# Kernel optimization log

Hardware: AMD Instinct MI355X
Metric: run time of the kernel (lower is better)

## Reference

```python
import jax, jax.numpy as jnp
import numpy as np

N = 100000
E = 1600000
IN_C, HID_C, OUT_C = 128, 128, 64


def setup_inputs() -> dict:
    key = jax.random.key(0)
    ks = jax.random.split(key, 8)
    x = jax.random.normal(ks[0], (N, IN_C), dtype=jnp.float32)
    edge_index = jax.random.randint(ks[1], (2, E), 0, N, dtype=jnp.int64)
    s = 1.0 / np.sqrt(IN_C)
    s2 = 1.0 / np.sqrt(HID_C)
    return {
        "x": x,
        "edge_index": edge_index,
        # layer 1: SAGEConv(in=128, out=128): lin_l (neighbor, with bias), lin_r (root, no bias)
        "W_l1": jax.random.uniform(ks[2], (IN_C, HID_C), jnp.float32, -s, s),
        "b_l1": jnp.zeros((HID_C,), jnp.float32),
        "W_r1": jax.random.uniform(ks[3], (IN_C, HID_C), jnp.float32, -s, s),
        # layer 2: SAGEConv(in=128, out=64)
        "W_l2": jax.random.uniform(ks[4], (HID_C, OUT_C), jnp.float32, -s2, s2),
        "b_l2": jnp.zeros((OUT_C,), jnp.float32),
        "W_r2": jax.random.uniform(ks[5], (HID_C, OUT_C), jnp.float32, -s2, s2),
    }


def _sage_conv(x, src, dst, W_l, b_l, W_r, n_nodes):
    # mean aggregation of source-node features at target nodes
    msg = x[src]                                    # [E, d] gather
    agg = jax.ops.segment_sum(msg, dst, num_segments=n_nodes)          # [N, d]
    cnt = jax.ops.segment_sum(jnp.ones((src.shape[0], 1), x.dtype), dst,
                              num_segments=n_nodes)                    # [N, 1]
    mean = agg / jnp.maximum(cnt, 1.0)
    # out = lin_l(mean_neighbors) + lin_r(x_self)
    return mean @ W_l + b_l + x @ W_r


def reference(x, edge_index, W_l1, b_l1, W_r1, W_l2, b_l2, W_r2):
    src, dst = edge_index[0], edge_index[1]
    n = x.shape[0]
    h = _sage_conv(x, src, dst, W_l1, b_l1, W_r1, n)
    h = jax.nn.relu(h)  # dropout is identity in eval mode
    out = _sage_conv(h, src, dst, W_l2, b_l2, W_r2, n)
    return out
```

## Files before the change

kernel.cpp:

```cpp
#include <hip/hip_runtime.h>
#include <hip/hip_bf16.h>
#include <stdint.h>

#define IN_C 128
#define HID_C 128
#define OUT_C 64

#define NBUCK 256
#define BSH 9
#define EPB 4096

typedef _Float16 h8 __attribute__((ext_vector_type(8)));
typedef _Float16 h2 __attribute__((ext_vector_type(2)));
typedef float f4 __attribute__((ext_vector_type(4)));
typedef float f2 __attribute__((ext_vector_type(2)));
typedef unsigned u4 __attribute__((ext_vector_type(4)));

__device__ inline float h2lo(unsigned v){ h2 t = __builtin_bit_cast(h2, v); return (float)t[0]; }
__device__ inline float h2hi(unsigned v){ h2 t = __builtin_bit_cast(h2, v); return (float)t[1]; }
__device__ inline unsigned packh2(float a, float b){ h2 t; t[0]=(_Float16)a; t[1]=(_Float16)b; return __builtin_bit_cast(unsigned, t); }

__global__ __launch_bounds__(256) void k_hist(const int* __restrict__ dst, int E,
                                              int* __restrict__ histT, int NBLK){
    __shared__ int h[NBUCK];
    int t = threadIdx.x;
    h[t] = 0; __syncthreads();
    int e0 = blockIdx.x*EPB, e1 = min(E, e0 + EPB);
    for (int e = e0 + t; e < e1; e += 256) atomicAdd(&h[((unsigned)dst[e]) >> BSH], 1);
    __syncthreads();
    histT[t*NBLK + blockIdx.x] = h[t];
}

__global__ void k_scanA(const int* __restrict__ cnt, int* __restrict__ tmp, int* __restrict__ bsum, int n){
    __shared__ int s[256];
    int t = threadIdx.x, g = blockIdx.x*256 + t;
    int v = (g < n) ? cnt[g] : 0;
    s[t] = v; __syncthreads();
    for (int off = 1; off < 256; off <<= 1){
        int a = (t >= off) ? s[t-off] : 0;
        __syncthreads();
        s[t] += a;
        __syncthreads();
    }
    int excl = (t == 0) ? 0 : s[t-1];
    if (g < n) tmp[g] = excl;
    if (t == 255) bsum[blockIdx.x] = s[255];
}

__global__ void k_scanB(int* __restrict__ bsum, int nb){
    __shared__ int s[1024];
    int t = threadIdx.x;
    int v = (t < nb) ? bsum[t] : 0;
    s[t] = v; __syncthreads();
    for (int off = 1; off < 1024; off <<= 1){
        int a = (t >= off) ? s[t-off] : 0;
        __syncthreads();
        s[t] += a;
        __syncthreads();
    }
    int excl = (t == 0) ? 0 : s[t-1];
    if (t < nb) bsum[t] = excl;
}

__global__ __launch_bounds__(256) void k_scatter(const int* __restrict__ src, const int* __restrict__ dst,
                                                 int E, const int* __restrict__ tmp, const int* __restrict__ bsum,
                                                 int NBLK, unsigned* __restrict__ sorted){
    __shared__ int off[NBUCK];
    int t = threadIdx.x;
    int g = t*NBLK + blockIdx.x;
    off[t] = tmp[g] + bsum[g >> 8];
    __syncthreads();
    int e0 = blockIdx.x*EPB, e1 = min(E, e0 + EPB);
    for (int e = e0 + t; e < e1; e += 256){
        int d = dst[e];
        int b = ((unsigned)d) >> BSH;
        int p = atomicAdd(&off[b], 1);
        sorted[p] = (unsigned)src[e] | (((unsigned)(d & ((1<<BSH)-1))) << 17);
    }
}

__global__ __launch_bounds__(512) void k_csr(const unsigned* __restrict__ sorted,
                                             const int* __restrict__ tmp, const int* __restrict__ bsum,
                                             int NBLK, int E, int N,
                                             int* __restrict__ csr, int* __restrict__ row_start){
    __shared__ int cnt[512];
    __shared__ int sc[512];
    int b = blockIdx.x, t = threadIdx.x;
    int i0 = b*NBLK;
    int bs = tmp[i0] + bsum[i0 >> 8];
    int be = (b == NBUCK-1) ? E : (tmp[i0 + NBLK] + bsum[(i0 + NBLK) >> 8]);
    cnt[t] = 0; __syncthreads();
    for (int e = bs + t; e < be; e += 512) atomicAdd(&cnt[sorted[e] >> 17], 1);
    __syncthreads();
    sc[t] = cnt[t]; __syncthreads();
    for (int off = 1; off < 512; off <<= 1){
        int a = (t >= off) ? sc[t-off] : 0;
        __syncthreads();
        sc[t] += a;
        __syncthreads();
    }
    int excl = sc[t] - cnt[t];
    int nid = (b << BSH) + t;
    if (nid < N) row_start[nid] = bs + excl;
    if (t == 0 && b == (N >> BSH)) row_start[N] = E;
    __syncthreads();
    cnt[t] = excl;
    __syncthreads();
    for (int e = bs + t; e < be; e += 512){
        unsigned v = sorted[e];
        int dl = v >> 17;
        int p = atomicAdd(&cnt[dl], 1);
        csr[bs + p] = (int)(v & 0x1FFFFu);
    }
}

__global__ void k_cvt(const float* __restrict__ x, h8* __restrict__ xh, uint2* __restrict__ x8, int n8){
    int g = blockIdx.x*256 + threadIdx.x;
    if (g < n8){
        const f4* xp = (const f4*)(x + (size_t)g*8);
        f4 a = xp[0], b = xp[1];
        h8 o;
        o[0]=(_Float16)a[0]; o[1]=(_Float16)a[1]; o[2]=(_Float16)a[2]; o[3]=(_Float16)a[3];
        o[4]=(_Float16)b[0]; o[5]=(_Float16)b[1]; o[6]=(_Float16)b[2]; o[7]=(_Float16)b[3];
        xh[g] = o;
        int w0 = __builtin_amdgcn_cvt_pk_fp8_f32(a[0], a[1], 0, false);
        w0     = __builtin_amdgcn_cvt_pk_fp8_f32(a[2], a[3], w0, true);
        int w1 = __builtin_amdgcn_cvt_pk_fp8_f32(b[0], b[1], 0, false);
        w1     = __builtin_amdgcn_cvt_pk_fp8_f32(b[2], b[3], w1, true);
        uint2 p; p.x = (unsigned)w0; p.y = (unsigned)w1;
        x8[g] = p;
    }
}

__device__ inline void pack_one(const float* __restrict__ W, int C, _Float16* __restrict__ outp, int tid){
    int l = tid & 63;
    int f = tid >> 6;
    int NJT = C / 16;
    int kt = f / NJT;
    int jt = f - kt*NJT;
    int kbase = kt*32 + (l >> 4)*8;
    int col   = jt*16 + (l & 15);
    h8 o;
    #pragma unroll
    for (int r = 0; r < 8; ++r) o[r] = (_Float16)W[(kbase + r)*C + col];
    ((h8*)outp)[f*64 + l] = o;
}

__global__ void k_pack(const float* __restrict__ Wl1, const float* __restrict__ Wr1,
                       const float* __restrict__ Wl2, const float* __restrict__ Wr2,
                       _Float16* __restrict__ wl1p, _Float16* __restrict__ wr1p,
                       _Float16* __restrict__ wl2p, _Float16* __restrict__ wr2p){
    int tid = blockIdx.x*256 + threadIdx.x;
    if (tid < 2048)        pack_one(Wl1, 128, wl1p, tid);
    else if (tid < 4096)   pack_one(Wr1, 128, wr1p, tid - 2048);
    else if (tid < 5120)   pack_one(Wl2,  64, wl2p, tid - 4096);
    else if (tid < 6144)   pack_one(Wr2,  64, wr2p, tid - 5120);
}

__global__ void k_agg1(const int* __restrict__ row_start, const int* __restrict__ csr,
                       const uint2* __restrict__ x8, unsigned* __restrict__ mh32, int n){
    int node = (int)((blockIdx.x*(unsigned)blockDim.x + threadIdx.x) >> 4);
    int c = threadIdx.x & 15;
    if (node >= n) return;
    int base = row_start[node], end = row_start[node+1];
    int deg = end - base;
    f2 a0={0.f,0.f}, a1={0.f,0.f}, a2={0.f,0.f}, a3={0.f,0.f};
    f2 b0={0.f,0.f}, b1={0.f,0.f}, b2={0.f,0.f}, b3={0.f,0.f};
    int i = base;
    for (; i + 3 < end; i += 4){
        int e0 = csr[i], e1 = csr[i+1], e2 = csr[i+2], e3 = csr[i+3];
        uint2 v0 = x8[(size_t)e0*16 + c];
        uint2 v1 = x8[(size_t)e1*16 + c];
        uint2 v2 = x8[(size_t)e2*16 + c];
        uint2 v3 = x8[(size_t)e3*16 + c];
        a0 += __builtin_amdgcn_cvt_pk_f32_fp8(v0.x, false);
        a1 += __builtin_amdgcn_cvt_pk_f32_fp8(v0.x, true);
        a2 += __builtin_amdgcn_cvt_pk_f32_fp8(v0.y, false);
        a3 += __builtin_amdgcn_cvt_pk_f32_fp8(v0.y, true);
        b0 += __builtin_amdgcn_cvt_pk_f32_fp8(v1.x, false);
        b1 += __builtin_amdgcn_cvt_pk_f32_fp8(v1.x, true);
        b2 += __builtin_amdgcn_cvt_pk_f32_fp8(v1.y, false);
        b3 += __builtin_amdgcn_cvt_pk_f32_fp8(v1.y, true);
        a0 += __builtin_amdgcn_cvt_pk_f32_fp8(v2.x, false);
        a1 += __builtin_amdgcn_cvt_pk_f32_fp8(v2.x, true);
        a2 += __builtin_amdgcn_cvt_pk_f32_fp8(v2.y, false);
        a3 += __builtin_amdgcn_cvt_pk_f32_fp8(v2.y, true);
        b0 += __builtin_amdgcn_cvt_pk_f32_fp8(v3.x, false);
        b1 += __builtin_amdgcn_cvt_pk_f32_fp8(v3.x, true);
        b2 += __builtin_amdgcn_cvt_pk_f32_fp8(v3.y, false);
        b3 += __builtin_amdgcn_cvt_pk_f32_fp8(v3.y, true);
    }
    for (; i < end; ++i){
        int e = csr[i];
        uint2 v = x8[(size_t)e*16 + c];
        a0 += __builtin_amdgcn_cvt_pk_f32_fp8(v.x, false);
        a1 += __builtin_amdgcn_cvt_pk_f32_fp8(v.x, true);
        a2 += __builtin_amdgcn_cvt_pk_f32_fp8(v.y, false);
        a3 += __builtin_amdgcn_cvt_pk_f32_fp8(v.y, true);
    }
    a0 += b0; a1 += b1; a2 += b2; a3 += b3;
    float sc = 1.0f / (float)max(deg, 1);
    u4 o;
    o[0] = packh2(a0[0]*sc, a0[1]*sc);
    o[1] = packh2(a1[0]*sc, a1[1]*sc);
    o[2] = packh2(a2[0]*sc, a2[1]*sc);
    o[3] = packh2(a3[0]*sc, a3[1]*sc);
    *(u4*)(mh32 + (size_t)node*64 + 4*c) = o;
}

__global__ __launch_bounds__(256, 2) void k_gemm_fused(
    const _Float16* __restrict__ A0,
    const _Float16* __restrict__ A1,
    const h8* __restrict__ B0,
    const h8* __restrict__ B1,
    const float* __restrict__ bias1,
    const h8* __restrict__ W2l,
    const h8* __restrict__ W2r,
    const float* __restrict__ bias2,
    unsigned* __restrict__ P8,
    float* __restrict__ Q,
    int M)
{
    __shared__ h8 shB[4096];
    int tid = threadIdx.x;
    #pragma unroll
    for (int i = 0; i < 8; ++i) shB[i*256 + tid] = B0[i*256 + tid];
    #pragma unroll
    for (int i = 0; i < 8; ++i) shB[2048 + i*256 + tid] = B1[i*256 + tid];
    __syncthreads();

    int wid = tid >> 6, lane = tid & 63;
    int m0 = (blockIdx.x*4 + wid) * 16;
    if (m0 >= M) return;
    int m = lane & 15, kg = lane >> 4;
    int rowc = min(m0 + m, M-1);

    f4 acc[8];
    #pragma unroll
    for (int j = 0; j < 8; ++j) acc[j] = (f4)0.0f;

    #pragma unroll
    for (int ph = 0; ph < 2; ++ph){
        const _Float16* A = ph ? A1 : A0;
        #pragma unroll
        for (int kt = 0; kt < 4; ++kt){
            h8 nf = *(const h8*)(A + (size_t)rowc*128 + kt*32 + kg*8);
            #pragma unroll
            for (int j = 0; j < 8; ++j){
                h8 wf = shB[ph*2048 + (kt*8 + j)*64 + lane];
                acc[j] = __builtin_amdgcn_mfma_f32_16x16x32_f16(wf, nf, acc[j], 0, 0, 0);
            }
        }
    }

    unsigned hreg[16];
    #pragma unroll
    for (int j = 0; j < 8; ++j){
        f4 bb = *(const f4*)(bias1 + j*16 + kg*4);
        float v0 = acc[j][0] + bb[0]; v0 = v0 > 0.f ? v0 : 0.f;
        float v1 = acc[j][1] + bb[1]; v1 = v1 > 0.f ? v1 : 0.f;
        float v2 = acc[j][2] + bb[2]; v2 = v2 > 0.f ? v2 : 0.f;
        float v3 = acc[j][3] + bb[3]; v3 = v3 > 0.f ? v3 : 0.f;
        hreg[2*j]   = packh2(v0, v1);
        hreg[2*j+1] = packh2(v2, v3);
    }

    f4 accP[4], accQ[4];
    #pragma unroll
    for (int j = 0; j < 4; ++j){ accP[j] = (f4)0.0f; accQ[j] = (f4)0.0f; }

    int srcA = ((kg & 1) * 2) * 16 + m;
    int srcB = srcA + 16;
    bool hi = (kg >> 1) & 1;

    #pragma unroll
    for (int kt = 0; kt < 4; ++kt){
        unsigned sA0 = (unsigned)__shfl((int)hreg[4*kt+0], srcA, 64);
        unsigned sA1 = (unsigned)__shfl((int)hreg[4*kt+1], srcA, 64);
        unsigned sA2 = (unsigned)__shfl((int)hreg[4*kt+2], srcA, 64);
        unsigned sA3 = (unsigned)__shfl((int)hreg[4*kt+3], srcA, 64);
        unsigned sB0 = (unsigned)__shfl((int)hreg[4*kt+0], srcB, 64);
        unsigned sB1 = (unsigned)__shfl((int)hreg[4*kt+1], srcB, 64);
        unsigned sB2 = (unsigned)__shfl((int)hreg[4*kt+2], srcB, 64);
        unsigned sB3 = (unsigned)__shfl((int)hreg[4*kt+3], srcB, 64);
        u4 u;
        u[0] = hi ? sA2 : sA0;
        u[1] = hi ? sA3 : sA1;
        u[2] = hi ? sB2 : sB0;
        u[3] = hi ? sB3 : sB1;
        h8 hf = __builtin_bit_cast(h8, u);
        #pragma unroll
        for (int j2 = 0; j2 < 4; ++j2){
            accP[j2] = __builtin_amdgcn_mfma_f32_16x16x32_f16(W2l[(kt*4 + j2)*64 + lane], hf, accP[j2], 0, 0, 0);
            accQ[j2] = __builtin_amdgcn_mfma_f32_16x16x32_f16(W2r[(kt*4 + j2)*64 + lane], hf, accQ[j2], 0, 0, 0);
        }
    }

    int node = m0 + m;
    if (node < M){
        #pragma unroll
        for (int j2 = 0; j2 < 4; ++j2){
            int f = j2*16 + kg*4;
            int p8 = __builtin_amdgcn_cvt_pk_fp8_f32(accP[j2][0], accP[j2][1], 0, false);
            p8     = __builtin_amdgcn_cvt_pk_fp8_f32(accP[j2][2], accP[j2][3], p8, true);
            P8[(size_t)node*16 + j2*4 + kg] = (unsigned)p8;
            f4 bb2 = *(const f4*)(bias2 + f);
            f4 qv;
            qv[0] = accQ[j2][0] + bb2[0];
            qv[1] = accQ[j2][1] + bb2[1];
            qv[2] = accQ[j2][2] + bb2[2];
            qv[3] = accQ[j2][3] + bb2[3];
            *(f4*)(Q + (size_t)node*64 + f) = qv;
        }
    }
}

__global__ void k_agg2f(const int* __restrict__ row_start, const int* __restrict__ csr,
                        const unsigned* __restrict__ p8, const float* __restrict__ Q,
                        float* __restrict__ out, int n){
    int node = (int)((blockIdx.x*(unsigned)blockDim.x + threadIdx.x) >> 4);
    int c = threadIdx.x & 15;
    if (node >= n) return;
    int base = row_start[node], end = row_start[node+1];
    int deg = end - base;
    f2 a0={0.f,0.f}, a1={0.f,0.f}, b0={0.f,0.f}, b1={0.f,0.f};
    f2 c0={0.f,0.f}, c1={0.f,0.f}, d0={0.f,0.f}, d1={0.f,0.f};
    int i = base;
    for (; i + 3 < end; i += 4){
        int e0 = csr[i], e1 = csr[i+1], e2 = csr[i+2], e3 = csr[i+3];
        unsigned v0 = p8[(size_t)e0*16 + c];
        unsigned v1 = p8[(size_t)e1*16 + c];
        unsigned v2 = p8[(size_t)e2*16 + c];
        unsigned v3 = p8[(size_t)e3*16 + c];
        a0 += __builtin_amdgcn_cvt_pk_f32_fp8(v0, false);
        a1 += __builtin_amdgcn_cvt_pk_f32_fp8(v0, true);
        b0 += __builtin_amdgcn_cvt_pk_f32_fp8(v1, false);
        b1 += __builtin_amdgcn_cvt_pk_f32_fp8(v1, true);
        c0 += __builtin_amdgcn_cvt_pk_f32_fp8(v2, false);
        c1 += __builtin_amdgcn_cvt_pk_f32_fp8(v2, true);
        d0 += __builtin_amdgcn_cvt_pk_f32_fp8(v3, false);
        d1 += __builtin_amdgcn_cvt_pk_f32_fp8(v3, true);
    }
    for (; i < end; ++i){
        int e = csr[i];
        unsigned v = p8[(size_t)e*16 + c];
        a0 += __builtin_amdgcn_cvt_pk_f32_fp8(v, false);
        a1 += __builtin_amdgcn_cvt_pk_f32_fp8(v, true);
    }
    a0 += b0 + c0 + d0;
    a1 += b1 + c1 + d1;
    float sc = 1.0f / (float)max(deg, 1);
    f4 q = *(const f4*)(Q + (size_t)node*64 + 4*c);
    f4 o;
    o[0] = a0[0]*sc + q[0];
    o[1] = a0[1]*sc + q[1];
    o[2] = a1[0]*sc + q[2];
    o[3] = a1[1]*sc + q[3];
    *(f4*)(out + (size_t)node*64 + 4*c) = o;
}

extern "C" void kernel_launch(void* const* d_in, const int* in_sizes, int n_in,
                              void* d_out, int out_size, void* d_ws, size_t ws_size,
                              hipStream_t stream) {
    const float* x   = (const float*)d_in[0];
    const int*   ei  = (const int*)d_in[1];
    const float* Wl1 = (const float*)d_in[2];
    const float* bl1 = (const float*)d_in[3];
    const float* Wr1 = (const float*)d_in[4];
    const float* Wl2 = (const float*)d_in[5];
    const float* bl2 = (const float*)d_in[6];
    const float* Wr2 = (const float*)d_in[7];

    const int N = in_sizes[0] / IN_C;
    const int E = in_sizes[1] / 2;
    const int* src = ei;
    const int* dst = ei + E;

    const int NBLK = (E + EPB - 1) / EPB;
    const int n_s  = NBUCK * NBLK;

    char* w = (char*)d_ws;
    size_t off = 0;
    auto alloc = [&](size_t bytes) -> char* {
        char* p = w + off;
        off = (off + bytes + 255) & ~(size_t)255;
        return p;
    };
    int* histT      = (int*)alloc((size_t)n_s*4);
    int* tmp        = (int*)alloc((size_t)n_s*4);
    int* bsum       = (int*)alloc(4096);
    unsigned* sorted= (unsigned*)alloc((size_t)E*4);
    int* csr        = (int*)alloc((size_t)E*4);
    int* row_start  = (int*)alloc((size_t)(N+1)*4);
    _Float16* xh    = (_Float16*)alloc((size_t)N*IN_C*2);
    unsigned* x8    = (unsigned*)alloc((size_t)N*IN_C);
    _Float16* m1h   = (_Float16*)alloc((size_t)N*IN_C*2);
    unsigned* p8    = (unsigned*)alloc((size_t)N*OUT_C);
    _Float16* wl1p  = (_Float16*)alloc(4*8*64*8*2);
    _Float16* wr1p  = (_Float16*)alloc(4*8*64*8*2);
    _Float16* wl2p  = (_Float16*)alloc(4*4*64*8*2);
    _Float16* wr2p  = (_Float16*)alloc(4*4*64*8*2);

    const int SB = (n_s + 255) / 256;

    k_hist   <<<NBLK, 256, 0, stream>>>(dst, E, histT, NBLK);
    k_scanA  <<<SB, 256, 0, stream>>>(histT, tmp, bsum, n_s);
    k_scanB  <<<1, 1024, 0, stream>>>(bsum, SB);
    k_scatter<<<NBLK, 256, 0, stream>>>(src, dst, E, tmp, bsum, NBLK, sorted);
    k_csr    <<<NBUCK, 512, 0, stream>>>(sorted, tmp, bsum, NBLK, E, N, csr, row_start);

    const int n8 = N*IN_C/8;
    k_cvt<<<(n8 + 255)/256, 256, 0, stream>>>(x, (h8*)xh, (uint2*)x8, n8);
    k_pack<<<24, 256, 0, stream>>>(Wl1, Wr1, Wl2, Wr2, wl1p, wr1p, wl2p, wr2p);

    const int AB = (N + 15) / 16;
    k_agg1<<<AB, 256, 0, stream>>>(row_start, csr, (const uint2*)x8, (unsigned*)m1h, N);

    float* Q = (float*)d_out;
    const int GB2 = (N + 63)/64;
    k_gemm_fused<<<GB2, 256, 0, stream>>>(m1h, xh, (const h8*)wl1p, (const h8*)wr1p, bl1,
                                          (const h8*)wl2p, (const h8*)wr2p, bl2,
                                          p8, Q, N);

    k_agg2f<<<AB, 256, 0, stream>>>(row_start, csr, p8, Q, (float*)d_out, N);
}
```

Before: 159.8 us.

## Fuse front-end kernels, split neighbor edges across lanes, store Q in fp16

Histogram, weight packing and the fp32-to-fp16/fp8 conversion are merged into one launch, which removes two kernel launches. EPB is doubled, so there are fewer histogram and scatter blocks, and scanB shrinks to 256 threads. Both aggregation kernels now give each wave four nodes in turn, with the four 16-lane groups reading different edges in parallel and combining results by cross-lane shuffles, which exposes more memory parallelism per node. The layer-2 root term Q is stored as fp16 in workspace instead of fp32 in the output, which halves that traffic but lowers precision.

```diff
diff --git a/kernel.cpp b/kernel.cpp
--- a/kernel.cpp
+++ b/kernel.cpp
@@ -8,7 +8,7 @@
 
 #define NBUCK 256
 #define BSH 9
-#define EPB 4096
+#define EPB 8192
 
 typedef _Float16 h8 __attribute__((ext_vector_type(8)));
 typedef _Float16 h2 __attribute__((ext_vector_type(2)));
@@ -20,15 +20,59 @@
 __device__ inline float h2hi(unsigned v){ h2 t = __builtin_bit_cast(h2, v); return (float)t[1]; }
 __device__ inline unsigned packh2(float a, float b){ h2 t; t[0]=(_Float16)a; t[1]=(_Float16)b; return __builtin_bit_cast(unsigned, t); }
 
-__global__ __launch_bounds__(256) void k_hist(const int* __restrict__ dst, int E,
-                                              int* __restrict__ histT, int NBLK){
+__device__ inline void pack_one(const float* __restrict__ W, int C, _Float16* __restrict__ outp, int tid){
+    int l = tid & 63;
+    int f = tid >> 6;
+    int NJT = C / 16;
+    int kt = f / NJT;
+    int jt = f - kt*NJT;
+    int kbase = kt*32 + (l >> 4)*8;
+    int col   = jt*16 + (l & 15);
+    h8 o;
+    #pragma unroll
+    for (int r = 0; r < 8; ++r) o[r] = (_Float16)W[(kbase + r)*C + col];
+    ((h8*)outp)[f*64 + l] = o;
+}
+
+__global__ __launch_bounds__(256) void k_front(const int* __restrict__ dst, int E, int NBLK,
+                                               int* __restrict__ histT,
+                                               const float* __restrict__ x, h8* __restrict__ xh,
+                                               uint2* __restrict__ x8, int n8,
+                                               const float* __restrict__ Wl1, const float* __restrict__ Wr1,
+                                               const float* __restrict__ Wl2, const float* __restrict__ Wr2,
+                                               _Float16* __restrict__ wl1p, _Float16* __restrict__ wr1p,
+                                               _Float16* __restrict__ wl2p, _Float16* __restrict__ wr2p){
     __shared__ int h[NBUCK];
-    int t = threadIdx.x;
-    h[t] = 0; __syncthreads();
-    int e0 = blockIdx.x*EPB, e1 = min(E, e0 + EPB);
-    for (int e = e0 + t; e < e1; e += 256) atomicAdd(&h[((unsigned)dst[e]) >> BSH], 1);
-    __syncthreads();
-    histT[t*NBLK + blockIdx.x] = h[t];
+    int bid = blockIdx.x, t = threadIdx.x;
+    if (bid < NBLK){
+        h[t] = 0; __syncthreads();
+        int e0 = bid*EPB, e1 = min(E, e0 + EPB);
+        for (int e = e0 + t; e < e1; e += 256) atomicAdd(&h[((unsigned)dst[e]) >> BSH], 1);
+        __syncthreads();
+        histT[t*NBLK + bid] = h[t];
+    } else if (bid < NBLK + 24){
+        int tid = (bid - NBLK)*256 + t;
+        if (tid < 2048)        pack_one(Wl1, 128, wl1p, tid);
+        else if (tid < 4096)   pack_one(Wr1, 128, wr1p, tid - 2048);
+        else if (tid < 5120)   pack_one(Wl2,  64, wl2p, tid - 4096);
+        else if (tid < 6144)   pack_one(Wr2,  64, wr2p, tid - 5120);
+    } else {
+        int g = (bid - NBLK - 24)*256 + t;
+        if (g < n8){
+            const f4* xp = (const f4*)(x + (size_t)g*8);
+            f4 a = xp[0], b = xp[1];
+            h8 o;
+            o[0]=(_Float16)a[0]; o[1]=(_Float16)a[1]; o[2]=(_Float16)a[2]; o[3]=(_Float16)a[3];
+            o[4]=(_Float16)b[0]; o[5]=(_Float16)b[1]; o[6]=(_Float16)b[2]; o[7]=(_Float16)b[3];
+            xh[g] = o;
+            int w0 = __builtin_amdgcn_cvt_pk_fp8_f32(a[0], a[1], 0, false);
+            w0     = __builtin_amdgcn_cvt_pk_fp8_f32(a[2], a[3], w0, true);
+            int w1 = __builtin_amdgcn_cvt_pk_fp8_f32(b[0], b[1], 0, false);
+            w1     = __builtin_amdgcn_cvt_pk_fp8_f32(b[2], b[3], w1, true);
+            uint2 p; p.x = (unsigned)w0; p.y = (unsigned)w1;
+            x8[g] = p;
+        }
+    }
 }
 
 __global__ void k_scanA(const int* __restrict__ cnt, int* __restrict__ tmp, int* __restrict__ bsum, int n){
@@ -48,11 +92,11 @@
 }
 
 __global__ void k_scanB(int* __restrict__ bsum, int nb){
-    __shared__ int s[1024];
+    __shared__ int s[256];
     int t = threadIdx.x;
     int v = (t < nb) ? bsum[t] : 0;
     s[t] = v; __syncthreads();
-    for (int off = 1; off < 1024; off <<= 1){
+    for (int off = 1; off < 256; off <<= 1){
         int a = (t >= off) ? s[t-off] : 0;
         __syncthreads();
         s[t] += a;
@@ -114,98 +158,65 @@
     }
 }
 
-__global__ void k_cvt(const float* __restrict__ x, h8* __restrict__ xh, uint2* __restrict__ x8, int n8){
-    int g = blockIdx.x*256 + threadIdx.x;
-    if (g < n8){
-        const f4* xp = (const f4*)(x + (size_t)g*8);
-        f4 a = xp[0], b = xp[1];
-        h8 o;
-        o[0]=(_Float16)a[0]; o[1]=(_Float16)a[1]; o[2]=(_Float16)a[2]; o[3]=(_Float16)a[3];
-        o[4]=(_Float16)b[0]; o[5]=(_Float16)b[1]; o[6]=(_Float16)b[2]; o[7]=(_Float16)b[3];
-        xh[g] = o;
-        int w0 = __builtin_amdgcn_cvt_pk_fp8_f32(a[0], a[1], 0, false);
-        w0     = __builtin_amdgcn_cvt_pk_fp8_f32(a[2], a[3], w0, true);
-        int w1 = __builtin_amdgcn_cvt_pk_fp8_f32(b[0], b[1], 0, false);
-        w1     = __builtin_amdgcn_cvt_pk_fp8_f32(b[2], b[3], w1, true);
-        uint2 p; p.x = (unsigned)w0; p.y = (unsigned)w1;
-        x8[g] = p;
-    }
-}
-
-__device__ inline void pack_one(const float* __restrict__ W, int C, _Float16* __restrict__ outp, int tid){
-    int l = tid & 63;
-    int f = tid >> 6;
-    int NJT = C / 16;
-    int kt = f / NJT;
-    int jt = f - kt*NJT;
-    int kbase = kt*32 + (l >> 4)*8;
-    int col   = jt*16 + (l & 15);
-    h8 o;
-    #pragma unroll
-    for (int r = 0; r < 8; ++r) o[r] = (_Float16)W[(kbase + r)*C + col];
-    ((h8*)outp)[f*64 + l] = o;
-}
-
-__global__ void k_pack(const float* __restrict__ Wl1, const float* __restrict__ Wr1,
-                       const float* __restrict__ Wl2, const float* __restrict__ Wr2,
-                       _Float16* __restrict__ wl1p, _Float16* __restrict__ wr1p,
-                       _Float16* __restrict__ wl2p, _Float16* __restrict__ wr2p){
-    int tid = blockIdx.x*256 + threadIdx.x;
-    if (tid < 2048)        pack_one(Wl1, 128, wl1p, tid);
-    else if (tid < 4096)   pack_one(Wr1, 128, wr1p, tid - 2048);
-    else if (tid < 5120)   pack_one(Wl2,  64, wl2p, tid - 4096);
-    else if (tid < 6144)   pack_one(Wr2,  64, wr2p, tid - 5120);
-}
-
-__global__ void k_agg1(const int* __restrict__ row_start, const int* __restrict__ csr,
-                       const uint2* __restrict__ x8, unsigned* __restrict__ mh32, int n){
-    int node = (int)((blockIdx.x*(unsigned)blockDim.x + threadIdx.x) >> 4);
-    int c = threadIdx.x & 15;
-    if (node >= n) return;
-    int base = row_start[node], end = row_start[node+1];
-    int deg = end - base;
-    f2 a0={0.f,0.f}, a1={0.f,0.f}, a2={0.f,0.f}, a3={0.f,0.f};
-    f2 b0={0.f,0.f}, b1={0.f,0.f}, b2={0.f,0.f}, b3={0.f,0.f};
-    int i = base;
-    for (; i + 3 < end; i += 4){
-        int e0 = csr[i], e1 = csr[i+1], e2 = csr[i+2], e3 = csr[i+3];
-        uint2 v0 = x8[(size_t)e0*16 + c];
-        uint2 v1 = x8[(size_t)e1*16 + c];
-        uint2 v2 = x8[(size_t)e2*16 + c];
-        uint2 v3 = x8[(size_t)e3*16 + c];
-        a0 += __builtin_amdgcn_cvt_pk_f32_fp8(v0.x, false);
-        a1 += __builtin_amdgcn_cvt_pk_f32_fp8(v0.x, true);
-        a2 += __builtin_amdgcn_cvt_pk_f32_fp8(v0.y, false);
-        a3 += __builtin_amdgcn_cvt_pk_f32_fp8(v0.y, true);
-        b0 += __builtin_amdgcn_cvt_pk_f32_fp8(v1.x, false);
-        b1 += __builtin_amdgcn_cvt_pk_f32_fp8(v1.x, true);
-        b2 += __builtin_amdgcn_cvt_pk_f32_fp8(v1.y, false);
-        b3 += __builtin_amdgcn_cvt_pk_f32_fp8(v1.y, true);
-        a0 += __builtin_amdgcn_cvt_pk_f32_fp8(v2.x, false);
-        a1 += __builtin_amdgcn_cvt_pk_f32_fp8(v2.x, true);
-        a2 += __builtin_amdgcn_cvt_pk_f32_fp8(v2.y, false);
-        a3 += __builtin_amdgcn_cvt_pk_f32_fp8(v2.y, true);
-        b0 += __builtin_amdgcn_cvt_pk_f32_fp8(v3.x, false);
-        b1 += __builtin_amdgcn_cvt_pk_f32_fp8(v3.x, true);
-        b2 += __builtin_amdgcn_cvt_pk_f32_fp8(v3.y, false);
-        b3 += __builtin_amdgcn_cvt_pk_f32_fp8(v3.y, true);
-    }
-    for (; i < end; ++i){
-        int e = csr[i];
-        uint2 v = x8[(size_t)e*16 + c];
-        a0 += __builtin_amdgcn_cvt_pk_f32_fp8(v.x, false);
-        a1 += __builtin_amdgcn_cvt_pk_f32_fp8(v.x, true);
-        a2 += __builtin_amdgcn_cvt_pk_f32_fp8(v.y, false);
-        a3 += __builtin_amdgcn_cvt_pk_f32_fp8(v.y, true);
-    }
-    a0 += b0; a1 += b1; a2 += b2; a3 += b3;
-    float sc = 1.0f / (float)max(deg, 1);
-    u4 o;
-    o[0] = packh2(a0[0]*sc, a0[1]*sc);
-    o[1] = packh2(a1[0]*sc, a1[1]*sc);
-    o[2] = packh2(a2[0]*sc, a2[1]*sc);
-    o[3] = packh2(a3[0]*sc, a3[1]*sc);
-    *(u4*)(mh32 + (size_t)node*64 + 4*c) = o;
+__global__ __launch_bounds__(256) void k_agg1(const int* __restrict__ row_start, const int* __restrict__ csr,
+                                              const uint2* __restrict__ x8, unsigned* __restrict__ mh32, int n){
+    int wave = (int)((blockIdx.x*(unsigned)blockDim.x + threadIdx.x) >> 6);
+    int lane = threadIdx.x & 63;
+    int e4 = lane >> 4, c = lane & 15;
+    int n0 = wave*4;
+    if (n0 >= n) return;
+    #pragma unroll 1
+    for (int k = 0; k < 4; ++k){
+        int node = n0 + k;
+        if (node >= n) break;
+        int base = row_start[node], end = row_start[node+1];
+        int deg = end - base;
+        f2 a0={0.f,0.f},a1={0.f,0.f},a2={0.f,0.f},a3={0.f,0.f};
+        f2 b0={0.f,0.f},b1={0.f,0.f},b2={0.f,0.f},b3={0.f,0.f};
+        int i = base;
+        for (; i + 8 <= end; i += 8){
+            int ea = csr[i + e4];
+            int eb = csr[i + 4 + e4];
+            uint2 va = x8[(size_t)ea*16 + c];
+            uint2 vb = x8[(size_t)eb*16 + c];
+            a0 += __builtin_amdgcn_cvt_pk_f32_fp8(va.x, false);
+            a1 += __builtin_amdgcn_cvt_pk_f32_fp8(va.x, true);
+            a2 += __builtin_amdgcn_cvt_pk_f32_fp8(va.y, false);
+            a3 += __builtin_amdgcn_cvt_pk_f32_fp8(va.y, true);
+            b0 += __builtin_amdgcn_cvt_pk_f32_fp8(vb.x, false);
+            b1 += __builtin_amdgcn_cvt_pk_f32_fp8(vb.x, true);
+            b2 += __builtin_amdgcn_cvt_pk_f32_fp8(vb.y, false);
+            b3 += __builtin_amdgcn_cvt_pk_f32_fp8(vb.y, true);
+        }
+        for (; i < end; i += 4){
+            if (i + e4 < end){
+                int e = csr[i + e4];
+                uint2 v = x8[(size_t)e*16 + c];
+                a0 += __builtin_amdgcn_cvt_pk_f32_fp8(v.x, false);
+                a1 += __builtin_amdgcn_cvt_pk_f32_fp8(v.x, true);
+                a2 += __builtin_amdgcn_cvt_pk_f32_fp8(v.y, false);
+                a3 += __builtin_amdgcn_cvt_pk_f32_fp8(v.y, true);
+            }
+        }
+        a0 += b0; a1 += b1; a2 += b2; a3 += b3;
+        a0[0] += __shfl_xor(a0[0], 16); a0[1] += __shfl_xor(a0[1], 16);
+        a1[0] += __shfl_xor(a1[0], 16); a1[1] += __shfl_xor(a1[1], 16);
+        a2[0] += __shfl_xor(a2[0], 16); a2[1] += __shfl_xor(a2[1], 16);
+        a3[0] += __shfl_xor(a3[0], 16); a3[1] += __shfl_xor(a3[1], 16);
+        a0[0] += __shfl_xor(a0[0], 32); a0[1] += __shfl_xor(a0[1], 32);
+        a1[0] += __shfl_xor(a1[0], 32); a1[1] += __shfl_xor(a1[1], 32);
+        a2[0] += __shfl_xor(a2[0], 32); a2[1] += __shfl_xor(a2[1], 32);
+        a3[0] += __shfl_xor(a3[0], 32); a3[1] += __shfl_xor(a3[1], 32);
+        if (e4 == 0){
+            float sc = 1.0f / (float)max(deg, 1);
+            u4 o;
+            o[0] = packh2(a0[0]*sc, a0[1]*sc);
+            o[1] = packh2(a1[0]*sc, a1[1]*sc);
+            o[2] = packh2(a2[0]*sc, a2[1]*sc);
+            o[3] = packh2(a3[0]*sc, a3[1]*sc);
+            *(u4*)(mh32 + (size_t)node*64 + 4*c) = o;
+        }
+    }
 }
 
 __global__ __launch_bounds__(256, 2) void k_gemm_fused(
@@ -218,7 +229,7 @@
     const h8* __restrict__ W2r,
     const float* __restrict__ bias2,
     unsigned* __restrict__ P8,
-    float* __restrict__ Q,
+    uint2* __restrict__ Qh,
     int M)
 {
     __shared__ h8 shB[4096];
@@ -305,58 +316,64 @@
             p8     = __builtin_amdgcn_cvt_pk_fp8_f32(accP[j2][2], accP[j2][3], p8, true);
             P8[(size_t)node*16 + j2*4 + kg] = (unsigned)p8;
             f4 bb2 = *(const f4*)(bias2 + f);
-            f4 qv;
-            qv[0] = accQ[j2][0] + bb2[0];
-            qv[1] = accQ[j2][1] + bb2[1];
-            qv[2] = accQ[j2][2] + bb2[2];
-            qv[3] = accQ[j2][3] + bb2[3];
-            *(f4*)(Q + (size_t)node*64 + f) = qv;
-        }
-    }
-}
-
-__global__ void k_agg2f(const int* __restrict__ row_start, const int* __restrict__ csr,
-                        const unsigned* __restrict__ p8, const float* __restrict__ Q,
-                        float* __restrict__ out, int n){
-    int node = (int)((blockIdx.x*(unsigned)blockDim.x + threadIdx.x) >> 4);
-    int c = threadIdx.x & 15;
-    if (node >= n) return;
-    int base = row_start[node], end = row_start[node+1];
-    int deg = end - base;
-    f2 a0={0.f,0.f}, a1={0.f,0.f}, b0={0.f,0.f}, b1={0.f,0.f};
-    f2 c0={0.f,0.f}, c1={0.f,0.f}, d0={0.f,0.f}, d1={0.f,0.f};
-    int i = base;
-    for (; i + 3 < end; i += 4){
-        int e0 = csr[i], e1 = csr[i+1], e2 = csr[i+2], e3 = csr[i+3];
-        unsigned v0 = p8[(size_t)e0*16 + c];
-        unsigned v1 = p8[(size_t)e1*16 + c];
-        unsigned v2 = p8[(size_t)e2*16 + c];
-        unsigned v3 = p8[(size_t)e3*16 + c];
-        a0 += __builtin_amdgcn_cvt_pk_f32_fp8(v0, false);
-        a1 += __builtin_amdgcn_cvt_pk_f32_fp8(v0, true);
-        b0 += __builtin_amdgcn_cvt_pk_f32_fp8(v1, false);
-        b1 += __builtin_amdgcn_cvt_pk_f32_fp8(v1, true);
-        c0 += __builtin_amdgcn_cvt_pk_f32_fp8(v2, false);
-        c1 += __builtin_amdgcn_cvt_pk_f32_fp8(v2, true);
-        d0 += __builtin_amdgcn_cvt_pk_f32_fp8(v3, false);
-        d1 += __builtin_amdgcn_cvt_pk_f32_fp8(v3, true);
-    }
-    for (; i < end; ++i){
-        int e = csr[i];
-        unsigned v = p8[(size_t)e*16 + c];
-        a0 += __builtin_amdgcn_cvt_pk_f32_fp8(v, false);
-        a1 += __builtin_amdgcn_cvt_pk_f32_fp8(v, true);
-    }
-    a0 += b0 + c0 + d0;
-    a1 += b1 + c1 + d1;
-    float sc = 1.0f / (float)max(deg, 1);
-    f4 q = *(const f4*)(Q + (size_t)node*64 + 4*c);
-    f4 o;
-    o[0] = a0[0]*sc + q[0];
-    o[1] = a0[1]*sc + q[1];
-    o[2] = a1[0]*sc + q[2];
-    o[3] = a1[1]*sc + q[3];
-    *(f4*)(out + (size_t)node*64 + 4*c) = o;
+            uint2 qp;
+            qp.x = packh2(accQ[j2][0] + bb2[0], accQ[j2][1] + bb2[1]);
+            qp.y = packh2(accQ[j2][2] + bb2[2], accQ[j2][3] + bb2[3]);
+            Qh[(size_t)node*16 + j2*4 + kg] = qp;
+        }
+    }
+}
+
+__global__ __launch_bounds__(256) void k_agg2f(const int* __restrict__ row_start, const int* __restrict__ csr,
+                                               const unsigned* __restrict__ p8, const uint2* __restrict__ Qh,
+                                               float* __restrict__ out, int n){
+    int wave = (int)((blockIdx.x*(unsigned)blockDim.x + threadIdx.x) >> 6);
+    int lane = threadIdx.x & 63;
+    int e4 = lane >> 4, c = lane & 15;
+    int n0 = wave*4;
+    if (n0 >= n) return;
+    #pragma unroll 1
+    for (int k = 0; k < 4; ++k){
+        int node = n0 + k;
+        if (node >= n) break;
+        int base = row_start[node], end = row_start[node+1];
+        int deg = end - base;
+        f2 a0={0.f,0.f}, a1={0.f,0.f}, b0={0.f,0.f}, b1={0.f,0.f};
+        int i = base;
+        for (; i + 8 <= end; i += 8){
+            int ea = csr[i + e4];
+            int eb = csr[i + 4 + e4];
+            unsigned va = p8[(size_t)ea*16 + c];
+            unsigned vb = p8[(size_t)eb*16 + c];
+            a0 += __builtin_amdgcn_cvt_pk_f32_fp8(va, false);
+            a1 += __builtin_amdgcn_cvt_pk_f32_fp8(va, true);
+            b0 += __builtin_amdgcn_cvt_pk_f32_fp8(vb, false);
+            b1 += __builtin_amdgcn_cvt_pk_f32_fp8(vb, true);
+        }
+        for (; i < end; i += 4){
+            if (i + e4 < end){
+                int e = csr[i + e4];
+                unsigned v = p8[(size_t)e*16 + c];
+                a0 += __builtin_amdgcn_cvt_pk_f32_fp8(v, false);
+                a1 += __builtin_amdgcn_cvt_pk_f32_fp8(v, true);
+            }
+        }
+        a0 += b0; a1 += b1;
+        a0[0] += __shfl_xor(a0[0], 16); a0[1] += __shfl_xor(a0[1], 16);
+        a1[0] += __shfl_xor(a1[0], 16); a1[1] += __shfl_xor(a1[1], 16);
+        a0[0] += __shfl_xor(a0[0], 32); a0[1] += __shfl_xor(a0[1], 32);
+        a1[0] += __shfl_xor(a1[0], 32); a1[1] += __shfl_xor(a1[1], 32);
+        if (e4 == 0){
+            float sc = 1.0f / (float)max(deg, 1);
+            uint2 qh = Qh[(size_t)node*16 + c];
+            f4 o;
+            o[0] = a0[0]*sc + h2lo(qh.x);
+            o[1] = a0[1]*sc + h2hi(qh.x);
+            o[2] = a1[0]*sc + h2lo(qh.y);
+            o[3] = a1[1]*sc + h2hi(qh.y);
+            *(f4*)(out + (size_t)node*64 + 4*c) = o;
+        }
+    }
 }
 
 extern "C" void kernel_launch(void* const* d_in, const int* in_sizes, int n_in,
@@ -396,31 +413,31 @@
     unsigned* x8    = (unsigned*)alloc((size_t)N*IN_C);
     _Float16* m1h   = (_Float16*)alloc((size_t)N*IN_C*2);
     unsigned* p8    = (unsigned*)alloc((size_t)N*OUT_C);
+    unsigned* qh    = (unsigned*)alloc((size_t)N*OUT_C*2);
     _Float16* wl1p  = (_Float16*)alloc(4*8*64*8*2);
     _Float16* wr1p  = (_Float16*)alloc(4*8*64*8*2);
     _Float16* wl2p  = (_Float16*)alloc(4*4*64*8*2);
     _Float16* wr2p  = (_Float16*)alloc(4*4*64*8*2);
 
     const int SB = (n_s + 255) / 256;
-
-    k_hist   <<<NBLK, 256, 0, stream>>>(dst, E, histT, NBLK);
+    const int n8 = N*IN_C/8;
+    const int CVB = (n8 + 255)/256;
+
+    k_front  <<<NBLK + 24 + CVB, 256, 0, stream>>>(dst, E, NBLK, histT,
+                                                   x, (h8*)xh, (uint2*)x8, n8,
+                                                   Wl1, Wr1, Wl2, Wr2, wl1p, wr1p, wl2p, wr2p);
     k_scanA  <<<SB, 256, 0, stream>>>(histT, tmp, bsum, n_s);
-    k_scanB  <<<1, 1024, 0, stream>>>(bsum, SB);
+    k_scanB  <<<1, 256, 0, stream>>>(bsum, SB);
     k_scatter<<<NBLK, 256, 0, stream>>>(src, dst, E, tmp, bsum, NBLK, sorted);
     k_csr    <<<NBUCK, 512, 0, stream>>>(sorted, tmp, bsum, NBLK, E, N, csr, row_start);
 
-    const int n8 = N*IN_C/8;
-    k_cvt<<<(n8 + 255)/256, 256, 0, stream>>>(x, (h8*)xh, (uint2*)x8, n8);
-    k_pack<<<24, 256, 0, stream>>>(Wl1, Wr1, Wl2, Wr2, wl1p, wr1p, wl2p, wr2p);
-
-    const int AB = (N + 15) / 16;
-    k_agg1<<<AB, 256, 0, stream>>>(row_start, csr, (const uint2*)x8, (unsigned*)m1h, N);
-
-    float* Q = (float*)d_out;
+    const int AGB = (N + 15) / 16;
+    k_agg1<<<AGB, 256, 0, stream>>>(row_start, csr, (const uint2*)x8, (unsigned*)m1h, N);
+
     const int GB2 = (N + 63)/64;
     k_gemm_fused<<<GB2, 256, 0, stream>>>(m1h, xh, (const h8*)wl1p, (const h8*)wr1p, bl1,
                                           (const h8*)wl2p, (const h8*)wr2p, bl2,
-                                          p8, Q, N);
-
-    k_agg2f<<<AB, 256, 0, stream>>>(row_start, csr, p8, Q, (float*)d_out, N);
-}
+                                          p8, (uint2*)qh, N);
+
+    k_agg2f<<<AGB, 256, 0, stream>>>(row_start, csr, p8, (const uint2*)qh, (float*)d_out, N);
+}
```

New measurement: 188.6 us. +18.0%, slower.

## Merge histogram, convert and pack into one launch; store root term in fp16

Applied to the files above, without the earlier changes.

Combines the edge histogram, the input fp16/fp8 conversion and the weight packing into a single k_front launch with block-range dispatch, cutting two kernel launches and letting them overlap. Doubles edges per histogram block, which halves the histogram size and lets the block-sum scan run in 256 threads. Stores the layer-2 root projection Q as fp16 in workspace instead of fp32 in the output buffer, halving its write and read traffic at the cost of extra rounding error in the final output.

```diff
diff --git a/kernel.cpp b/kernel.cpp
--- a/kernel.cpp
+++ b/kernel.cpp
@@ -8,7 +8,7 @@
 
 #define NBUCK 256
 #define BSH 9
-#define EPB 4096
+#define EPB 8192
 
 typedef _Float16 h8 __attribute__((ext_vector_type(8)));
 typedef _Float16 h2 __attribute__((ext_vector_type(2)));
@@ -20,15 +20,59 @@
 __device__ inline float h2hi(unsigned v){ h2 t = __builtin_bit_cast(h2, v); return (float)t[1]; }
 __device__ inline unsigned packh2(float a, float b){ h2 t; t[0]=(_Float16)a; t[1]=(_Float16)b; return __builtin_bit_cast(unsigned, t); }
 
-__global__ __launch_bounds__(256) void k_hist(const int* __restrict__ dst, int E,
-                                              int* __restrict__ histT, int NBLK){
+__device__ inline void pack_one(const float* __restrict__ W, int C, _Float16* __restrict__ outp, int tid){
+    int l = tid & 63;
+    int f = tid >> 6;
+    int NJT = C / 16;
+    int kt = f / NJT;
+    int jt = f - kt*NJT;
+    int kbase = kt*32 + (l >> 4)*8;
+    int col   = jt*16 + (l & 15);
+    h8 o;
+    #pragma unroll
+    for (int r = 0; r < 8; ++r) o[r] = (_Float16)W[(kbase + r)*C + col];
+    ((h8*)outp)[f*64 + l] = o;
+}
+
+__global__ __launch_bounds__(256) void k_front(const int* __restrict__ dst, int E, int NBLK,
+                                               int* __restrict__ histT,
+                                               const float* __restrict__ x, h8* __restrict__ xh,
+                                               uint2* __restrict__ x8, int n8,
+                                               const float* __restrict__ Wl1, const float* __restrict__ Wr1,
+                                               const float* __restrict__ Wl2, const float* __restrict__ Wr2,
+                                               _Float16* __restrict__ wl1p, _Float16* __restrict__ wr1p,
+                                               _Float16* __restrict__ wl2p, _Float16* __restrict__ wr2p){
     __shared__ int h[NBUCK];
-    int t = threadIdx.x;
-    h[t] = 0; __syncthreads();
-    int e0 = blockIdx.x*EPB, e1 = min(E, e0 + EPB);
-    for (int e = e0 + t; e < e1; e += 256) atomicAdd(&h[((unsigned)dst[e]) >> BSH], 1);
-    __syncthreads();
-    histT[t*NBLK + blockIdx.x] = h[t];
+    int bid = blockIdx.x, t = threadIdx.x;
+    if (bid < NBLK){
+        h[t] = 0; __syncthreads();
+        int e0 = bid*EPB, e1 = min(E, e0 + EPB);
+        for (int e = e0 + t; e < e1; e += 256) atomicAdd(&h[((unsigned)dst[e]) >> BSH], 1);
+        __syncthreads();
+        histT[t*NBLK + bid] = h[t];
+    } else if (bid < NBLK + 24){
+        int tid = (bid - NBLK)*256 + t;
+        if (tid < 2048)        pack_one(Wl1, 128, wl1p, tid);
+        else if (tid < 4096)   pack_one(Wr1, 128, wr1p, tid - 2048);
+        else if (tid < 5120)   pack_one(Wl2,  64, wl2p, tid - 4096);
+        else if (tid < 6144)   pack_one(Wr2,  64, wr2p, tid - 5120);
+    } else {
+        int g = (bid - NBLK - 24)*256 + t;
+        if (g < n8){
+            const f4* xp = (const f4*)(x + (size_t)g*8);
+            f4 a = xp[0], b = xp[1];
+            h8 o;
+            o[0]=(_Float16)a[0]; o[1]=(_Float16)a[1]; o[2]=(_Float16)a[2]; o[3]=(_Float16)a[3];
+            o[4]=(_Float16)b[0]; o[5]=(_Float16)b[1]; o[6]=(_Float16)b[2]; o[7]=(_Float16)b[3];
+            xh[g] = o;
+            int w0 = __builtin_amdgcn_cvt_pk_fp8_f32(a[0], a[1], 0, false);
+            w0     = __builtin_amdgcn_cvt_pk_fp8_f32(a[2], a[3], w0, true);
+            int w1 = __builtin_amdgcn_cvt_pk_fp8_f32(b[0], b[1], 0, false);
+            w1     = __builtin_amdgcn_cvt_pk_fp8_f32(b[2], b[3], w1, true);
+            uint2 p; p.x = (unsigned)w0; p.y = (unsigned)w1;
+            x8[g] = p;
+        }
+    }
 }
 
 __global__ void k_scanA(const int* __restrict__ cnt, int* __restrict__ tmp, int* __restrict__ bsum, int n){
@@ -48,11 +92,11 @@
 }
 
 __global__ void k_scanB(int* __restrict__ bsum, int nb){
-    __shared__ int s[1024];
+    __shared__ int s[256];
     int t = threadIdx.x;
     int v = (t < nb) ? bsum[t] : 0;
     s[t] = v; __syncthreads();
-    for (int off = 1; off < 1024; off <<= 1){
+    for (int off = 1; off < 256; off <<= 1){
         int a = (t >= off) ? s[t-off] : 0;
         __syncthreads();
         s[t] += a;
@@ -112,49 +156,6 @@
         int p = atomicAdd(&cnt[dl], 1);
         csr[bs + p] = (int)(v & 0x1FFFFu);
     }
-}
-
-__global__ void k_cvt(const float* __restrict__ x, h8* __restrict__ xh, uint2* __restrict__ x8, int n8){
-    int g = blockIdx.x*256 + threadIdx.x;
-    if (g < n8){
-        const f4* xp = (const f4*)(x + (size_t)g*8);
-        f4 a = xp[0], b = xp[1];
-        h8 o;
-        o[0]=(_Float16)a[0]; o[1]=(_Float16)a[1]; o[2]=(_Float16)a[2]; o[3]=(_Float16)a[3];
-        o[4]=(_Float16)b[0]; o[5]=(_Float16)b[1]; o[6]=(_Float16)b[2]; o[7]=(_Float16)b[3];
-        xh[g] = o;
-        int w0 = __builtin_amdgcn_cvt_pk_fp8_f32(a[0], a[1], 0, false);
-        w0     = __builtin_amdgcn_cvt_pk_fp8_f32(a[2], a[3], w0, true);
-        int w1 = __builtin_amdgcn_cvt_pk_fp8_f32(b[0], b[1], 0, false);
-        w1     = __builtin_amdgcn_cvt_pk_fp8_f32(b[2], b[3], w1, true);
-        uint2 p; p.x = (unsigned)w0; p.y = (unsigned)w1;
-        x8[g] = p;
-    }
-}
-
-__device__ inline void pack_one(const float* __restrict__ W, int C, _Float16* __restrict__ outp, int tid){
-    int l = tid & 63;
-    int f = tid >> 6;
-    int NJT = C / 16;
-    int kt = f / NJT;
-    int jt = f - kt*NJT;
-    int kbase = kt*32 + (l >> 4)*8;
-    int col   = jt*16 + (l & 15);
-    h8 o;
-    #pragma unroll
-    for (int r = 0; r < 8; ++r) o[r] = (_Float16)W[(kbase + r)*C + col];
-    ((h8*)outp)[f*64 + l] = o;
-}
-
-__global__ void k_pack(const float* __restrict__ Wl1, const float* __restrict__ Wr1,
-                       const float* __restrict__ Wl2, const float* __restrict__ Wr2,
-                       _Float16* __restrict__ wl1p, _Float16* __restrict__ wr1p,
-                       _Float16* __restrict__ wl2p, _Float16* __restrict__ wr2p){
-    int tid = blockIdx.x*256 + threadIdx.x;
-    if (tid < 2048)        pack_one(Wl1, 128, wl1p, tid);
-    else if (tid < 4096)   pack_one(Wr1, 128, wr1p, tid - 2048);
-    else if (tid < 5120)   pack_one(Wl2,  64, wl2p, tid - 4096);
-    else if (tid < 6144)   pack_one(Wr2,  64, wr2p, tid - 5120);
 }
 
 __global__ void k_agg1(const int* __restrict__ row_start, const int* __restrict__ csr,
@@ -218,7 +219,7 @@
     const h8* __restrict__ W2r,
     const float* __restrict__ bias2,
     unsigned* __restrict__ P8,
-    float* __restrict__ Q,
+    uint2* __restrict__ Qh,
     int M)
 {
     __shared__ h8 shB[4096];
@@ -305,18 +306,16 @@
             p8     = __builtin_amdgcn_cvt_pk_fp8_f32(accP[j2][2], accP[j2][3], p8, true);
             P8[(size_t)node*16 + j2*4 + kg] = (unsigned)p8;
             f4 bb2 = *(const f4*)(bias2 + f);
-            f4 qv;
-            qv[0] = accQ[j2][0] + bb2[0];
-            qv[1] = accQ[j2][1] + bb2[1];
-            qv[2] = accQ[j2][2] + bb2[2];
-            qv[3] = accQ[j2][3] + bb2[3];
-            *(f4*)(Q + (size_t)node*64 + f) = qv;
+            uint2 qp;
+            qp.x = packh2(accQ[j2][0] + bb2[0], accQ[j2][1] + bb2[1]);
+            qp.y = packh2(accQ[j2][2] + bb2[2], accQ[j2][3] + bb2[3]);
+            Qh[(size_t)node*16 + j2*4 + kg] = qp;
         }
     }
 }
 
 __global__ void k_agg2f(const int* __restrict__ row_start, const int* __restrict__ csr,
-                        const unsigned* __restrict__ p8, const float* __restrict__ Q,
+                        const unsigned* __restrict__ p8, const uint2* __restrict__ Qh,
                         float* __restrict__ out, int n){
     int node = (int)((blockIdx.x*(unsigned)blockDim.x + threadIdx.x) >> 4);
     int c = threadIdx.x & 15;
@@ -350,12 +349,12 @@
     a0 += b0 + c0 + d0;
     a1 += b1 + c1 + d1;
     float sc = 1.0f / (float)max(deg, 1);
-    f4 q = *(const f4*)(Q + (size_t)node*64 + 4*c);
+    uint2 qh = Qh[(size_t)node*16 + c];
     f4 o;
-    o[0] = a0[0]*sc + q[0];
-    o[1] = a0[1]*sc + q[1];
-    o[2] = a1[0]*sc + q[2];
-    o[3] = a1[1]*sc + q[3];
+    o[0] = a0[0]*sc + h2lo(qh.x);
+    o[1] = a0[1]*sc + h2hi(qh.x);
+    o[2] = a1[0]*sc + h2lo(qh.y);
+    o[3] = a1[1]*sc + h2hi(qh.y);
     *(f4*)(out + (size_t)node*64 + 4*c) = o;
 }
 
@@ -396,31 +395,31 @@
     unsigned* x8    = (unsigned*)alloc((size_t)N*IN_C);
     _Float16* m1h   = (_Float16*)alloc((size_t)N*IN_C*2);
     unsigned* p8    = (unsigned*)alloc((size_t)N*OUT_C);
+    unsigned* qh    = (unsigned*)alloc((size_t)N*OUT_C*2);
     _Float16* wl1p  = (_Float16*)alloc(4*8*64*8*2);
     _Float16* wr1p  = (_Float16*)alloc(4*8*64*8*2);
     _Float16* wl2p  = (_Float16*)alloc(4*4*64*8*2);
     _Float16* wr2p  = (_Float16*)alloc(4*4*64*8*2);
 
     const int SB = (n_s + 255) / 256;
-
-    k_hist   <<<NBLK, 256, 0, stream>>>(dst, E, histT, NBLK);
+    const int n8 = N*IN_C/8;
+    const int CVB = (n8 + 255)/256;
+
+    k_front  <<<NBLK + 24 + CVB, 256, 0, stream>>>(dst, E, NBLK, histT,
+                                                   x, (h8*)xh, (uint2*)x8, n8,
+                                                   Wl1, Wr1, Wl2, Wr2, wl1p, wr1p, wl2p, wr2p);
     k_scanA  <<<SB, 256, 0, stream>>>(histT, tmp, bsum, n_s);
-    k_scanB  <<<1, 1024, 0, stream>>>(bsum, SB);
+    k_scanB  <<<1, 256, 0, stream>>>(bsum, SB);
     k_scatter<<<NBLK, 256, 0, stream>>>(src, dst, E, tmp, bsum, NBLK, sorted);
     k_csr    <<<NBUCK, 512, 0, stream>>>(sorted, tmp, bsum, NBLK, E, N, csr, row_start);
 
-    const int n8 = N*IN_C/8;
-    k_cvt<<<(n8 + 255)/256, 256, 0, stream>>>(x, (h8*)xh, (uint2*)x8, n8);
-    k_pack<<<24, 256, 0, stream>>>(Wl1, Wr1, Wl2, Wr2, wl1p, wr1p, wl2p, wr2p);
-
     const int AB = (N + 15) / 16;
     k_agg1<<<AB, 256, 0, stream>>>(row_start, csr, (const uint2*)x8, (unsigned*)m1h, N);
 
-    float* Q = (float*)d_out;
     const int GB2 = (N + 63)/64;
     k_gemm_fused<<<GB2, 256, 0, stream>>>(m1h, xh, (const h8*)wl1p, (const h8*)wr1p, bl1,
                                           (const h8*)wl2p, (const h8*)wr2p, bl2,
-                                          p8, Q, N);
-
-    k_agg2f<<<AB, 256, 0, stream>>>(row_start, csr, p8, Q, (float*)d_out, N);
-}
+                                          p8, (uint2*)qh, N);
+
+    k_agg2f<<<AB, 256, 0, stream>>>(row_start, csr, p8, (const uint2*)qh, (float*)d_out, N);
+}
```

After: 160.8 us. About the same (+0.7%).
